# Performance work log

Hardware: AMD Instinct MI355X
Metric: run time of the kernel (lower is better)

Reference implementation:

```python
import jax, jax.numpy as jnp
import numpy as np


def _conv2d(x, w, b, pad):
    out = jax.lax.conv_general_dilated(
        x, w, window_strides=(1, 1), padding=[(pad, pad), (pad, pad)],
        dimension_numbers=("NCHW", "OIHW", "NCHW"))
    return out + b[None, :, None, None]


def _bilinear_sample(x, py, px):
    # x: [B,C,H,W]; py, px: [B,K,H,W] float sample coords -> [B,C,K,H,W]
    B, C, H, W = x.shape
    y0 = jnp.floor(py)
    x0 = jnp.floor(px)
    y1 = y0 + 1.0
    x1 = x0 + 1.0
    wy1 = py - y0
    wy0 = 1.0 - wy1
    wx1 = px - x0
    wx0 = 1.0 - wx1
    xf = x.reshape(B, C, H * W)

    def corner(yc, xc, wgt):
        valid = (yc >= 0) & (yc <= H - 1) & (xc >= 0) & (xc <= W - 1)
        yi = jnp.clip(yc, 0, H - 1).astype(jnp.int32)
        xi = jnp.clip(xc, 0, W - 1).astype(jnp.int32)
        idx = yi * W + xi                      # [B,K,H,W]
        g = jax.vmap(lambda f, i: f[:, i.reshape(-1)])(xf, idx)  # [B,C,K*H*W]
        g = g.reshape(B, C, idx.shape[1], H, W)
        return g * (wgt * valid)[:, None]      # zero weight outside image

    return (corner(y0, x0, wy0 * wx0) + corner(y0, x1, wy0 * wx1)
            + corner(y1, x0, wy1 * wx0) + corner(y1, x1, wy1 * wx1))


def reference(x, c, w_off, b_off, w_dcn, b_dcn):
    # DCNv2Pack forward: conv_offset(c) -> (o1, o2, mask); modulated deform conv on x.
    B, C, H, W = x.shape
    pad, K = 1, 9
    off_out = _conv2d(c, w_off, b_off, pad)            # [B,27,H,W]
    o1, o2, m = jnp.split(off_out, 3, axis=1)
    offset = jnp.concatenate([o1, o2], axis=1)         # [B,18,H,W]
    mask = jax.nn.sigmoid(m)                           # [B,9,H,W]
    # offset channel layout: [dy_0, dx_0, dy_1, dx_1, ...] per kernel tap
    off = offset.reshape(B, K, 2, H, W)
    ky, kx = jnp.meshgrid(jnp.arange(3), jnp.arange(3), indexing="ij")
    ky = (ky.reshape(K) - pad).astype(x.dtype)
    kx = (kx.reshape(K) - pad).astype(x.dtype)
    base_y = jnp.arange(H, dtype=x.dtype).reshape(1, 1, H, 1)
    base_x = jnp.arange(W, dtype=x.dtype).reshape(1, 1, 1, W)
    py = base_y + ky.reshape(1, K, 1, 1) + off[:, :, 0]  # [B,K,H,W]
    px = base_x + kx.reshape(1, K, 1, 1) + off[:, :, 1]
    samp = _bilinear_sample(x, py, px)                 # [B,C,K,H,W]
    samp = samp * mask[:, None]                        # modulation
    C_out = w_dcn.shape[0]
    out = jnp.einsum("bckhw,ock->bohw", samp, w_dcn.reshape(C_out, C, K))
    return out + b_dcn[None, :, None, None]


def setup_inputs():
    key = jax.random.key(0)
    ks = jax.random.split(key, 4)
    B, C, H, W = 4, 64, 128, 128
    x = jax.random.normal(ks[0], (B, C, H, W), jnp.float32)
    c = jax.random.normal(ks[1], (B, C, H, W), jnp.float32)
    # conv_offset is zero-init in DCNv2Pack; use small random weights so
    # offsets are non-trivial but bounded (realistic trained regime).
    w_off = jax.random.normal(ks[2], (27, C, 3, 3), jnp.float32) * 0.01
    b_off = jnp.zeros((27,), jnp.float32)
    w_dcn = jax.random.normal(ks[3], (C, C, 3, 3), jnp.float32) * (1.0 / np.sqrt(C * 9))
    b_dcn = jnp.zeros((C,), jnp.float32)
    return {"x": x, "c": c, "w_off": w_off, "b_off": b_off,
            "w_dcn": w_dcn, "b_dcn": b_dcn}
```

## Files before the change

### kernel.cpp

```cpp
#include <hip/hip_runtime.h>
#include <math.h>

#define BB 4
#define C 64
#define H 128
#define W 128
#define HW (H*W)
#define KC 576
#define WROWS 8
#define WCOLS 40
#define CROWS 4
#define CCOLS 34

typedef __attribute__((ext_vector_type(4))) float f32x4;
typedef __attribute__((ext_vector_type(8))) _Float16 f16x8;

static __device__ __forceinline__ f16x8 splat8(float f) {
  _Float16 h = (_Float16)f;
  f16x8 v = {h, h, h, h, h, h, h, h};
  return v;
}

__global__ __launch_bounds__(256) void xpose_prep_kernel(
    const float* __restrict__ x, const float* __restrict__ cin,
    const float* __restrict__ wd, const float* __restrict__ woff,
    _Float16* __restrict__ xt, _Float16* __restrict__ ct,
    _Float16* __restrict__ wtbf, _Float16* __restrict__ wotf) {
  __shared__ _Float16 lds16[32 * 72];
  int t = threadIdx.x;

  if (blockIdx.y == 1 && blockIdx.x < 144) {
    int i = blockIdx.x * 256 + t;
    {
      int j = i & 7, ln = (i >> 3) & 63, fi = i >> 9;
      int ot = fi & 3, kb = fi >> 2;
      int o = ot * 16 + (ln & 15);
      int kcol = kb * 32 + (ln >> 4) * 8 + j;
      int k = kcol >> 6, cc = kcol & 63;
      wtbf[i] = (_Float16)wd[(o * C + cc) * 9 + k];
    }
    if (i < 32 * KC) {
      int j = i & 7, ln = (i >> 3) & 63, fi = i >> 9;
      int ot2 = fi & 1, kb = fi >> 1;
      int o = ot2 * 16 + (ln & 15);
      int kcol = kb * 32 + (ln >> 4) * 8 + j;
      int k = kcol >> 6, cc = kcol & 63;
      wotf[i] = (o < 27) ? (_Float16)woff[(o * C + cc) * 9 + k] : (_Float16)0.f;
    }
  }

  const float* src = blockIdx.y ? cin : x;
  _Float16* dst = blockIdx.y ? ct : xt;

  int P0 = blockIdx.x * 32;
  int b = P0 >> 14;
  int pp0 = P0 & (HW - 1);

  int p = t & 31;
  int cg = t >> 5;
  const float* xb = src + (size_t)b * C * HW + pp0 + p;
  f16x8 u;
#pragma unroll
  for (int j = 0; j < 8; ++j)
    u[j] = (_Float16)xb[(cg * 8 + j) * HW];
  *(f16x8*)(lds16 + p * 72 + ((cg ^ (p & 7)) << 3)) = u;

  __syncthreads();

  int q = t >> 3;
  int s = t & 7;
  f16x8 v = *(const f16x8*)(lds16 + q * 72 + ((s ^ (q & 7)) << 3));
  *(f16x8*)(dst + (size_t)(P0 + q) * 64 + s * 8) = v;
}

__global__ __launch_bounds__(256) void dcn_fused_kernel(
    const _Float16* __restrict__ xt, const _Float16* __restrict__ ct,
    const _Float16* __restrict__ wtbf, const _Float16* __restrict__ wotf,
    const float* __restrict__ boff, const float* __restrict__ bd,
    float* __restrict__ out) {
  __shared__ _Float16 win[WROWS * WCOLS * 64];
  __shared__ float offbuf[4][16][36];

  int tid = threadIdx.x;
  int bid = blockIdx.x;
  int w0 = (bid & 3) * 32;
  int h0 = ((bid >> 2) & 63) * 2;
  int b  = bid >> 8;

  int lane = tid & 63;
  int wv = tid >> 6;
  int lr = lane & 15, lh = lane >> 4;
  int h   = h0 + (wv >> 1);
  int wpx = w0 + (wv & 1) * 16 + lr;

  const _Float16* xtb = xt + (size_t)b * HW * 64;
  const _Float16* ctb = ct + (size_t)b * HW * 64;

  int crlo = min(max(h0 - 1, 0), H - CROWS);
  int cclo = min(max(w0 - 1, 0), W - CCOLS);
  int rlo  = min(max(h0 - 3, 0), H - WROWS);
  int clo  = min(max(w0 - 4, 0), W - WCOLS);

  auto rdwin = [&](int iy, int ix, int cg) -> f16x8 {
    int pix = iy * WCOLS + ix;
    return *(const f16x8*)(win + (size_t)pix * 64 + ((cg ^ (pix & 7)) << 3));
  };
  auto rdcwin = [&](int iy, int ix, int cg) -> f16x8 {
    int pix = iy * CCOLS + ix;
    return *(const f16x8*)(win + (size_t)pix * 64 + ((cg ^ (pix & 7)) << 3));
  };

#pragma unroll
  for (int sweep = 0; sweep < 5; ++sweep) {
    int cch = sweep * 256 + tid;
    if (cch < CROWS * CCOLS * 8) {
      int row = cch / (CCOLS * 8);
      int rem = cch - row * (CCOLS * 8);
      int col = rem >> 3, part = rem & 7;
      int pix = cch >> 3;
      *(f16x8*)(win + (size_t)pix * 64 + ((part ^ (pix & 7)) << 3)) =
        *(const f16x8*)(ctb + ((size_t)(crlo + row) * W + cclo + col) * 64 + part * 8);
    }
  }
  __syncthreads();

  f32x4 acc1a = {0.f, 0.f, 0.f, 0.f};
  f32x4 acc1b = {0.f, 0.f, 0.f, 0.f};
#pragma unroll 2
  for (int kb = 0; kb < 18; ++kb) {
    int t9 = kb >> 1;
    int cg = (kb & 1) * 4 + lh;
    int ty = h + t9 / 3 - 1;
    int tx = wpx + t9 % 3 - 1;
    bool okv = (ty >= 0) && (ty < H) && (tx >= 0) && (tx < W);
    int iy = min(max(ty, 0), H - 1) - crlo;
    int ix = min(max(tx, 0), W - 1) - cclo;
    f16x8 bf = rdcwin(iy, ix, cg);
    if (!okv) bf = splat8(0.f);
    f16x8 a0 = *(const f16x8*)(wotf + ((size_t)(kb * 2 + 0) * 64 + lane) * 8);
    f16x8 a1 = *(const f16x8*)(wotf + ((size_t)(kb * 2 + 1) * 64 + lane) * 8);
    acc1a = __builtin_amdgcn_mfma_f32_16x16x32_f16(a0, bf, acc1a, 0, 0, 0);
    acc1b = __builtin_amdgcn_mfma_f32_16x16x32_f16(a1, bf, acc1b, 0, 0, 0);
  }

  {
    f32x4 v0, v1;
#pragma unroll
    for (int r = 0; r < 4; ++r) {
      int o0 = lh * 4 + r;
      int o1 = 16 + lh * 4 + r;
      v0[r] = acc1a[r] + boff[o0];
      v1[r] = acc1b[r] + ((o1 < 27) ? boff[o1] : 0.f);
    }
    *(f32x4*)(&offbuf[wv][lr][lh * 4]) = v0;
    *(f32x4*)(&offbuf[wv][lr][16 + lh * 4]) = v1;
  }
  __syncthreads();

#pragma unroll
  for (int sweep = 0; sweep < 10; ++sweep) {
    int cch = sweep * 256 + tid;
    int row = cch / (WCOLS * 8);
    int rem = cch - row * (WCOLS * 8);
    int col = rem >> 3, part = rem & 7;
    int pix = cch >> 3;
    *(f16x8*)(win + (size_t)pix * 64 + ((part ^ (pix & 7)) << 3)) =
      *(const f16x8*)(xtb + ((size_t)(rlo + row) * W + clo + col) * 64 + part * 8);
  }
  __syncthreads();

  f32x4 acc[4];
#pragma unroll
  for (int i = 0; i < 4; ++i) acc[i] = (f32x4){0.f, 0.f, 0.f, 0.f};

#pragma unroll 1
  for (int k = 0; k < 9; ++k) {
    float dy = offbuf[wv][lr][2 * k];
    float dx = offbuf[wv][lr][2 * k + 1];
    float mv = offbuf[wv][lr][18 + k];
    float m = 1.0f / (1.0f + __expf(-mv));

    float py = (float)(h + k / 3 - 1) + dy;
    float px = (float)(wpx + k % 3 - 1) + dx;
    float y0f = floorf(py), x0f = floorf(px);
    int y0 = (int)y0f, x0 = (int)x0f;
    float wy1 = py - y0f, wx1 = px - x0f;
    float wy0 = 1.0f - wy1, wx0 = 1.0f - wx1;

    bool y0v = (y0 >= 0) && (y0 < H);
    bool y1v = (y0 + 1 >= 0) && (y0 + 1 < H);
    bool x0v = (x0 >= 0) && (x0 < W);
    bool x1v = (x0 + 1 >= 0) && (x0 + 1 < W);
    int y0c = min(max(y0, 0), H - 1), y1c = min(max(y0 + 1, 0), H - 1);
    int x0c = min(max(x0, 0), W - 1), x1c = min(max(x0 + 1, 0), W - 1);

    float w00 = wy0 * wx0 * (float)(y0v && x0v) * m;
    float w01 = wy0 * wx1 * (float)(y0v && x1v) * m;
    float w10 = wy1 * wx0 * (float)(y1v && x0v) * m;
    float w11 = wy1 * wx1 * (float)(y1v && x1v) * m;

    int iy0 = y0c - rlo, iy1 = y1c - rlo;
    int ix0 = x0c - clo, ix1 = x1c - clo;
    bool inY0 = (unsigned)iy0 < WROWS, inY1 = (unsigned)iy1 < WROWS;
    bool inX0 = (unsigned)ix0 < WCOLS, inX1 = (unsigned)ix1 < WCOLS;
    bool in00 = inY0 && inX0, in01 = inY0 && inX1;
    bool in10 = inY1 && inX0, in11 = inY1 && inX1;
    int jy0 = min(max(iy0, 0), WROWS - 1), jy1 = min(max(iy1, 0), WROWS - 1);
    int jx0 = min(max(ix0, 0), WCOLS - 1), jx1 = min(max(ix1, 0), WCOLS - 1);

#pragma unroll
    for (int half = 0; half < 2; ++half) {
      int cg = half * 4 + lh;
      f16x8 c00 = rdwin(jy0, jx0, cg);
      f16x8 c01 = rdwin(jy0, jx1, cg);
      f16x8 c10 = rdwin(jy1, jx0, cg);
      f16x8 c11 = rdwin(jy1, jx1, cg);
      if (!in00) c00 = *(const f16x8*)(xtb + ((size_t)y0c * W + x0c) * 64 + cg * 8);
      if (!in01) c01 = *(const f16x8*)(xtb + ((size_t)y0c * W + x1c) * 64 + cg * 8);
      if (!in10) c10 = *(const f16x8*)(xtb + ((size_t)y1c * W + x0c) * 64 + cg * 8);
      if (!in11) c11 = *(const f16x8*)(xtb + ((size_t)y1c * W + x1c) * 64 + cg * 8);

      f16x8 s = c00 * splat8(w00);
      s += c01 * splat8(w01);
      s += c10 * splat8(w10);
      s += c11 * splat8(w11);

      int kb = 2 * k + half;
#pragma unroll
      for (int ot = 0; ot < 4; ++ot) {
        f16x8 a = *(const f16x8*)(wtbf + ((size_t)(kb * 4 + ot) * 64 + lane) * 8);
        acc[ot] = __builtin_amdgcn_mfma_f32_16x16x32_f16(a, s, acc[ot], 0, 0, 0);
      }
    }
  }

#pragma unroll
  for (int ot = 0; ot < 4; ++ot) {
#pragma unroll
    for (int r = 0; r < 4; ++r) {
      int o = ot * 16 + lh * 4 + r;
      size_t base = ((size_t)(b * C + o)) * HW + (size_t)h * W + w0 + (wv & 1) * 16 + lr;
      out[base] = acc[ot][r] + bd[o];
    }
  }
}

extern "C" void kernel_launch(void* const* d_in, const int* in_sizes, int n_in,
                              void* d_out, int out_size, void* d_ws, size_t ws_size,
                              hipStream_t stream) {
  const float* x    = (const float*)d_in[0];
  const float* c    = (const float*)d_in[1];
  const float* woff = (const float*)d_in[2];
  const float* boff = (const float*)d_in[3];
  const float* wdcn = (const float*)d_in[4];
  const float* bdcn = (const float*)d_in[5];
  float* out = (float*)d_out;

  _Float16* xt   = (_Float16*)d_ws;
  _Float16* ct   = xt + 4194304;
  _Float16* wtbf = ct + 4194304;
  _Float16* wotf = wtbf + 36864;

  int npix = BB * H * W;
  dim3 gx(npix / 32, 2);
  xpose_prep_kernel<<<gx, 256, 0, stream>>>(x, c, wdcn, woff, xt, ct, wtbf, wotf);
  dcn_fused_kernel<<<npix / 64, 256, 0, stream>>>(xt, ct, wtbf, wotf, boff, bdcn, out);
}
```

Before: 42.60 us.

## Shrink x window, read offset-conv inputs from global, merge LDS buffers, unroll taps

Drops the LDS staging of the conditioning tile, so the offset-conv MFMA operands are read straight from global memory. The offset buffer now aliases the x-window LDS, and each lane copies its offsets into registers before the window is overwritten. The x window shrinks from 8x40 to 6x38 pixels to cut LDS footprint and staging traffic, and the 9-tap loop is fully unrolled. The aim is less LDS per block for higher occupancy, at the cost of more global fallback loads for samples outside the smaller window, more register pressure, and one extra barrier.

```diff
diff --git a/kernel.cpp b/kernel.cpp
--- a/kernel.cpp
+++ b/kernel.cpp
@@ -7,10 +7,8 @@
 #define W 128
 #define HW (H*W)
 #define KC 576
-#define WROWS 8
-#define WCOLS 40
-#define CROWS 4
-#define CCOLS 34
+#define XR 6
+#define XC 38
 
 typedef __attribute__((ext_vector_type(4))) float f32x4;
 typedef __attribute__((ext_vector_type(8))) _Float16 f16x8;
@@ -78,8 +76,8 @@
     const _Float16* __restrict__ wtbf, const _Float16* __restrict__ wotf,
     const float* __restrict__ boff, const float* __restrict__ bd,
     float* __restrict__ out) {
-  __shared__ _Float16 win[WROWS * WCOLS * 64];
-  __shared__ float offbuf[4][16][36];
+  __shared__ _Float16 win[XR * XC * 64];
+  float* offT = (float*)win;
 
   int tid = threadIdx.x;
   int bid = blockIdx.x;
@@ -96,33 +94,8 @@
   const _Float16* xtb = xt + (size_t)b * HW * 64;
   const _Float16* ctb = ct + (size_t)b * HW * 64;
 
-  int crlo = min(max(h0 - 1, 0), H - CROWS);
-  int cclo = min(max(w0 - 1, 0), W - CCOLS);
-  int rlo  = min(max(h0 - 3, 0), H - WROWS);
-  int clo  = min(max(w0 - 4, 0), W - WCOLS);
-
-  auto rdwin = [&](int iy, int ix, int cg) -> f16x8 {
-    int pix = iy * WCOLS + ix;
-    return *(const f16x8*)(win + (size_t)pix * 64 + ((cg ^ (pix & 7)) << 3));
-  };
-  auto rdcwin = [&](int iy, int ix, int cg) -> f16x8 {
-    int pix = iy * CCOLS + ix;
-    return *(const f16x8*)(win + (size_t)pix * 64 + ((cg ^ (pix & 7)) << 3));
-  };
-
-#pragma unroll
-  for (int sweep = 0; sweep < 5; ++sweep) {
-    int cch = sweep * 256 + tid;
-    if (cch < CROWS * CCOLS * 8) {
-      int row = cch / (CCOLS * 8);
-      int rem = cch - row * (CCOLS * 8);
-      int col = rem >> 3, part = rem & 7;
-      int pix = cch >> 3;
-      *(f16x8*)(win + (size_t)pix * 64 + ((part ^ (pix & 7)) << 3)) =
-        *(const f16x8*)(ctb + ((size_t)(crlo + row) * W + cclo + col) * 64 + part * 8);
-    }
-  }
-  __syncthreads();
+  int rlo = min(max(h0 - 2, 0), H - XR);
+  int clo = min(max(w0 - 3, 0), W - XC);
 
   f32x4 acc1a = {0.f, 0.f, 0.f, 0.f};
   f32x4 acc1b = {0.f, 0.f, 0.f, 0.f};
@@ -133,9 +106,8 @@
     int ty = h + t9 / 3 - 1;
     int tx = wpx + t9 % 3 - 1;
     bool okv = (ty >= 0) && (ty < H) && (tx >= 0) && (tx < W);
-    int iy = min(max(ty, 0), H - 1) - crlo;
-    int ix = min(max(tx, 0), W - 1) - cclo;
-    f16x8 bf = rdcwin(iy, ix, cg);
+    int yc = min(max(ty, 0), H - 1), xc = min(max(tx, 0), W - 1);
+    f16x8 bf = *(const f16x8*)(ctb + (size_t)(yc * W + xc) * 64 + cg * 8);
     if (!okv) bf = splat8(0.f);
     f16x8 a0 = *(const f16x8*)(wotf + ((size_t)(kb * 2 + 0) * 64 + lane) * 8);
     f16x8 a1 = *(const f16x8*)(wotf + ((size_t)(kb * 2 + 1) * 64 + lane) * 8);
@@ -152,20 +124,30 @@
       v0[r] = acc1a[r] + boff[o0];
       v1[r] = acc1b[r] + ((o1 < 27) ? boff[o1] : 0.f);
     }
-    *(f32x4*)(&offbuf[wv][lr][lh * 4]) = v0;
-    *(f32x4*)(&offbuf[wv][lr][16 + lh * 4]) = v1;
-  }
-  __syncthreads();
-
-#pragma unroll
-  for (int sweep = 0; sweep < 10; ++sweep) {
+    *(f32x4*)(offT + ((size_t)wv * 16 + lr) * 36 + lh * 4) = v0;
+    *(f32x4*)(offT + ((size_t)wv * 16 + lr) * 36 + 16 + lh * 4) = v1;
+  }
+  __syncthreads();
+
+  f32x4 rv[7];
+#pragma unroll
+  for (int j = 0; j < 7; ++j)
+    rv[j] = *(const f32x4*)(offT + ((size_t)wv * 16 + lr) * 36 + 4 * j);
+  __syncthreads();
+
+#define OFFV(i) (rv[(i) >> 2][(i) & 3])
+
+#pragma unroll
+  for (int sweep = 0; sweep < 8; ++sweep) {
     int cch = sweep * 256 + tid;
-    int row = cch / (WCOLS * 8);
-    int rem = cch - row * (WCOLS * 8);
-    int col = rem >> 3, part = rem & 7;
-    int pix = cch >> 3;
-    *(f16x8*)(win + (size_t)pix * 64 + ((part ^ (pix & 7)) << 3)) =
-      *(const f16x8*)(xtb + ((size_t)(rlo + row) * W + clo + col) * 64 + part * 8);
+    if (cch < XR * XC * 8) {
+      int row = cch / (XC * 8);
+      int rem = cch - row * (XC * 8);
+      int col = rem >> 3, part = rem & 7;
+      int pix = cch >> 3;
+      *(f16x8*)(win + (size_t)pix * 64 + ((part ^ (pix & 7)) << 3)) =
+        *(const f16x8*)(xtb + ((size_t)(rlo + row) * W + clo + col) * 64 + part * 8);
+    }
   }
   __syncthreads();
 
@@ -173,11 +155,11 @@
 #pragma unroll
   for (int i = 0; i < 4; ++i) acc[i] = (f32x4){0.f, 0.f, 0.f, 0.f};
 
-#pragma unroll 1
+#pragma unroll
   for (int k = 0; k < 9; ++k) {
-    float dy = offbuf[wv][lr][2 * k];
-    float dx = offbuf[wv][lr][2 * k + 1];
-    float mv = offbuf[wv][lr][18 + k];
+    float dy = OFFV(2 * k);
+    float dx = OFFV(2 * k + 1);
+    float mv = OFFV(18 + k);
     float m = 1.0f / (1.0f + __expf(-mv));
 
     float py = (float)(h + k / 3 - 1) + dy;
@@ -201,20 +183,22 @@
 
     int iy0 = y0c - rlo, iy1 = y1c - rlo;
     int ix0 = x0c - clo, ix1 = x1c - clo;
-    bool inY0 = (unsigned)iy0 < WROWS, inY1 = (unsigned)iy1 < WROWS;
-    bool inX0 = (unsigned)ix0 < WCOLS, inX1 = (unsigned)ix1 < WCOLS;
+    bool inY0 = (unsigned)iy0 < XR, inY1 = (unsigned)iy1 < XR;
+    bool inX0 = (unsigned)ix0 < XC, inX1 = (unsigned)ix1 < XC;
     bool in00 = inY0 && inX0, in01 = inY0 && inX1;
     bool in10 = inY1 && inX0, in11 = inY1 && inX1;
-    int jy0 = min(max(iy0, 0), WROWS - 1), jy1 = min(max(iy1, 0), WROWS - 1);
-    int jx0 = min(max(ix0, 0), WCOLS - 1), jx1 = min(max(ix1, 0), WCOLS - 1);
+    int p00 = min(max(iy0, 0), XR - 1) * XC + min(max(ix0, 0), XC - 1);
+    int p01 = min(max(iy0, 0), XR - 1) * XC + min(max(ix1, 0), XC - 1);
+    int p10 = min(max(iy1, 0), XR - 1) * XC + min(max(ix0, 0), XC - 1);
+    int p11 = min(max(iy1, 0), XR - 1) * XC + min(max(ix1, 0), XC - 1);
 
 #pragma unroll
     for (int half = 0; half < 2; ++half) {
       int cg = half * 4 + lh;
-      f16x8 c00 = rdwin(jy0, jx0, cg);
-      f16x8 c01 = rdwin(jy0, jx1, cg);
-      f16x8 c10 = rdwin(jy1, jx0, cg);
-      f16x8 c11 = rdwin(jy1, jx1, cg);
+      f16x8 c00 = *(const f16x8*)(win + (size_t)p00 * 64 + ((cg ^ (p00 & 7)) << 3));
+      f16x8 c01 = *(const f16x8*)(win + (size_t)p01 * 64 + ((cg ^ (p01 & 7)) << 3));
+      f16x8 c10 = *(const f16x8*)(win + (size_t)p10 * 64 + ((cg ^ (p10 & 7)) << 3));
+      f16x8 c11 = *(const f16x8*)(win + (size_t)p11 * 64 + ((cg ^ (p11 & 7)) << 3));
       if (!in00) c00 = *(const f16x8*)(xtb + ((size_t)y0c * W + x0c) * 64 + cg * 8);
       if (!in01) c01 = *(const f16x8*)(xtb + ((size_t)y0c * W + x1c) * 64 + cg * 8);
       if (!in10) c10 = *(const f16x8*)(xtb + ((size_t)y1c * W + x0c) * 64 + cg * 8);
```

Result: slower. 45.30 us (+6.3%).
